# Performance work log

Measured on AMD Instinct MI355X. Metric: run time of the kernel, lower is better.

Reference implementation:

```python
import jax, jax.numpy as jnp
import numpy as np

NUM_COMPONENTS = 8
STRIDE, PADDING, OUTPUT_PADDING, K = 2, 1, 0, 4


def get_comp_mat(n):
    # Cayley-Dickson construction: entry [i, j] = +/- component index of the
    # weight multiplying input component j to produce output component i.
    A = np.array([[0]])
    while A.shape[0] < n:
        m = A.shape[0]
        A = np.vstack([np.hstack([A, -(A + m)]), np.hstack([A + m, A])])
    return A


def setup_inputs() -> dict:
    key = jax.random.key(0)
    k1, k2, k3 = jax.random.split(key, 3)
    B, Cin, Cout, H = 8, 512, 256, 64
    c_in, c_out = Cin // NUM_COMPONENTS, Cout // NUM_COMPONENTS
    x = jax.random.normal(k1, (B, Cin, H, H), jnp.float32)
    # per-component ConvTranspose2d weights, torch layout [C_in, C_out, kH, kW]
    W = jax.random.normal(k2, (NUM_COMPONENTS, c_in, c_out, K, K), jnp.float32) * 0.05
    b = jax.random.normal(k3, (NUM_COMPONENTS, c_out), jnp.float32) * 0.05
    return {"x": x, "W": W, "b": b}


def reference(x, W, b):
    n = NUM_COMPONENTS
    comp = get_comp_mat(n)                 # static [n, n] signed component table
    signs = jnp.asarray(np.where(comp < 0, -1.0, 1.0), x.dtype)
    idx = np.abs(comp)                     # which sub-conv weight to use
    c_in, c_out, kh, kw = W.shape[1:]
    # Fuse the n^2 transpose convs into ONE block transpose conv:
    # Kbig[j*c_in:(j+1)*c_in, i*c_out:(i+1)*c_out] = sign[i,j] * W[idx[i,j]]
    Wsel = W[idx] * signs[:, :, None, None, None, None]          # [ni, nj, c_in, c_out, kh, kw]
    Wbig = jnp.transpose(Wsel, (1, 2, 0, 3, 4, 5)).reshape(n * c_in, n * c_out, kh, kw)
    bbig = jnp.einsum('ij,ijc->ic', signs, b[idx]).reshape(n * c_out)
    # torch ConvTranspose2d == conv with input dilated by stride and flipped kernel
    rhs = jnp.flip(Wbig, (2, 3)).transpose(1, 0, 2, 3)           # OIHW
    pad = K - 1 - PADDING
    out = jax.lax.conv_general_dilated(
        x, rhs, window_strides=(1, 1),
        padding=((pad, pad + OUTPUT_PADDING), (pad, pad + OUTPUT_PADDING)),
        lhs_dilation=(STRIDE, STRIDE),
        dimension_numbers=('NCHW', 'OIHW', 'NCHW'))
    return out + bbig[None, :, None, None]
```

## Files before the change

### kernel.cpp

```cpp
#include <hip/hip_runtime.h>
#include <hip/hip_bf16.h>

typedef unsigned short ushort_t;
typedef __attribute__((ext_vector_type(8))) short short8;
typedef __attribute__((ext_vector_type(4))) float f32x4;

#define NCOMP    8
#define CIN      512
#define COUT     256
#define H        64
#define HP       66
#define OHW      128
#define NB       8

__device__ const int d_idx8[8][8] = {
    {0,1,2,1,4,3,2,3},
    {1,0,3,2,5,4,1,2},
    {2,1,0,1,6,5,4,3},
    {3,2,1,0,7,6,5,4},
    {4,3,2,3,0,1,2,1},
    {5,4,1,2,1,0,3,2},
    {6,5,4,3,2,1,0,1},
    {7,6,5,4,3,2,1,0}};

__device__ const int kh_tab[2][2] = {{1,3},{0,2}};
__device__ const int dh_tab[2][2] = {{0,-1},{1,0}};

__global__ void zero_halo(ushort_t* __restrict__ xpadT) {
    const int t = blockIdx.x * 256 + threadIdx.x;
    const int nA = 8 * 2 * 66 * 64;
    short8 z = {0, 0, 0, 0, 0, 0, 0, 0};
    if (t < nA) {
        int v  = t & 63;
        int r  = t >> 6;
        int iw = r % 66;
        int q  = r / 66;
        int ih = (q & 1) * 65;
        int b  = q >> 1;
        *(short8*)(xpadT + (((size_t)b * HP + ih) * HP + iw) * CIN + v * 8) = z;
    } else {
        int u  = t - nA;
        int v  = u & 63;
        int r  = u >> 6;
        int e  = r & 1;
        int q  = r >> 1;
        int ih = (q & 63) + 1;
        int b  = q >> 6;
        int iw = e * 65;
        *(short8*)(xpadT + (((size_t)b * HP + ih) * HP + iw) * CIN + v * 8) = z;
    }
}

__global__ void prep_x(const float* __restrict__ x, ushort_t* __restrict__ xpadT) {
    __shared__ ushort_t tile[32][33];
    const int ih  = blockIdx.x;
    const int iw0 = (blockIdx.y & 1) * 32;
    const int ic0 = (blockIdx.y >> 1) * 32;
    const int b   = blockIdx.z;
    const int t   = threadIdx.x;

    for (int e = t; e < 1024; e += 256) {
        int icl = e >> 5, iwl = e & 31;
        float v = x[(((size_t)b * CIN + ic0 + icl) * H + ih) * H + iw0 + iwl];
        __hip_bfloat16 h = __float2bfloat16(v);
        tile[icl][iwl] = *(ushort_t*)&h;
    }
    __syncthreads();
    const int iwl = t >> 3, g = t & 7;
    ushort4 v;
    v.x = tile[g * 4 + 0][iwl];
    v.y = tile[g * 4 + 1][iwl];
    v.z = tile[g * 4 + 2][iwl];
    v.w = tile[g * 4 + 3][iwl];
    ushort_t* dst = xpadT + (((size_t)b * HP + ih + 1) * HP + iw0 + iwl + 1) * CIN + ic0 + g * 4;
    *(ushort4*)dst = v;
}

__global__ void prep_w(const float* __restrict__ W, const float* __restrict__ bias,
                       ushort_t* __restrict__ Abf, float* __restrict__ bbig) {
    const int t = blockIdx.x * blockDim.x + threadIdx.x;
    if (t < 4 * 64 * 256 * 32) {
        int kin = t & 31;
        int oc  = (t >> 5) & 255;
        int ks  = (t >> 13) & 63;
        int cls = t >> 19;
        int k  = ks * 32 + kin;
        int a  = k >> 10, c = (k >> 9) & 1, ic = k & 511;
        int ph = cls >> 1, pw = cls & 1;
        int kh = kh_tab[ph][a], kw = kh_tab[pw][c];
        int i = oc >> 5, co = oc & 31;
        int j = ic >> 6, ci = ic & 63;
        float s = (i >= j) ? 1.0f : -1.0f;
        float v = s * W[(((size_t)(d_idx8[i][j] * 64 + ci) * 32 + co) * 4 + kh) * 4 + kw];
        __hip_bfloat16 h = __float2bfloat16(v);
        Abf[t] = *(ushort_t*)&h;
    }
    if (t < COUT) {
        int i = t >> 5, co = t & 31;
        float acc = 0.0f;
        for (int j = 0; j < NCOMP; ++j)
            acc += ((i >= j) ? 1.0f : -1.0f) * bias[d_idx8[i][j] * 32 + co];
        bbig[t] = acc;
    }
}

__device__ __forceinline__ void async16(void* lds_dst, const void* g_src) {
    __builtin_amdgcn_global_load_lds(
        (const __attribute__((address_space(1))) unsigned int*)g_src,
        (__attribute__((address_space(3))) unsigned int*)lds_dst,
        16, 0, 0);
}

#define KSTEP(STEP, CB_CUR, CB_NXT)                                            \
  {                                                                            \
    const int ns = (STEP) + 1;                                                 \
    if (ns < 64) {                                                             \
      const int na  = ns >> 5;                                                 \
      const int ncb = (ns >> 4) & 1;                                           \
      const int go  = ((na ? dh1 : dh0) * HP + (ncb ? dw1 : dw0)) * CIN        \
                      + (ns & 15) * 32;                                        \
      const ushort_t* nap = Abf_t + (size_t)ns * 8192;                         \
      async16(sb + (CB_NXT) + t * 16,         nap);                            \
      async16(sb + (CB_NXT) + 4096 + t * 16,  nap + 2048);                     \
      async16(sb + (CB_NXT) + 8192 + t * 16,  base_r0 + go);                   \
      async16(sb + (CB_NXT) + 12288 + t * 16, base_r1 + go);                   \
    }                                                                          \
    short8 af[4], bf[4];                                                       \
    _Pragma("unroll")                                                          \
    for (int s = 0; s < 4; ++s) {                                              \
      af[s] = *(const short8*)(sb + (CB_CUR) + aoff + s * 1024);               \
      bf[s] = *(const short8*)(sb + (CB_CUR) + boff + s * 1024);               \
    }                                                                          \
    _Pragma("unroll")                                                          \
    for (int sm = 0; sm < 4; ++sm)                                             \
      _Pragma("unroll")                                                        \
      for (int sn = 0; sn < 4; ++sn)                                           \
        acc[sm][sn] = __builtin_amdgcn_mfma_f32_16x16x32_bf16(                 \
            af[sm], bf[sn], acc[sm][sn], 0, 0, 0);                             \
    asm volatile("s_waitcnt vmcnt(0) lgkmcnt(0)" ::: "memory");                \
    __builtin_amdgcn_s_barrier();                                              \
    __builtin_amdgcn_sched_barrier(0);                                         \
  }

__launch_bounds__(256)
__global__ void htconv_mfma(const ushort_t* __restrict__ xpadT,
                            const ushort_t* __restrict__ Abf,
                            const float* __restrict__ bbig,
                            float* __restrict__ out) {
    __shared__ __align__(16) ushort_t smem[16384];
    char* sb = (char*)smem;

    const int t     = threadIdx.x;
    const int ntile = blockIdx.x;
    const int mtile = blockIdx.y;
    const int cls   = blockIdx.z & 3;
    const int b     = blockIdx.z >> 2;
    const int ph = cls >> 1, pw = cls & 1;
    const int ohh0 = ntile * 2;

    const int srcc = (((t & 3) ^ ((t >> 3) & 3)) * 8);
    const int m_a  = t >> 2;
    const ushort_t* Abf_t =
        Abf + (((size_t)cls * 64) * 256 + (size_t)mtile * 128 + m_a) * 32 + srcc;

    const int dh0 = dh_tab[ph][0], dh1 = dh_tab[ph][1];
    const int dw0 = dh_tab[pw][0], dw1 = dh_tab[pw][1];
    const int oww = t >> 2;
    const ushort_t* base_r0 =
        xpadT + (((size_t)b * HP + ohh0 + 0 + 1) * HP + oww + 1) * CIN + srcc;
    const ushort_t* base_r1 =
        xpadT + (((size_t)b * HP + ohh0 + 1 + 1) * HP + oww + 1) * CIN + srcc;

    const int lane = t & 63, wave = t >> 6;
    const int wm = wave >> 1, wn = wave & 1;
    const int col = lane & 15, quad = lane >> 4;
    const int soff = (quad ^ ((col >> 1) & 3)) * 16;
    const int aoff = (wm * 64 + col) * 64 + soff;
    const int boff = 8192 + (wn * 64 + col) * 64 + soff;

    f32x4 acc[4][4];
#pragma unroll
    for (int i = 0; i < 4; ++i)
#pragma unroll
        for (int j = 0; j < 4; ++j)
            acc[i][j] = (f32x4){0.f, 0.f, 0.f, 0.f};

    {
        const int go0 = (dh0 * HP + dw0) * CIN;
        async16(sb + t * 16,         Abf_t);
        async16(sb + 4096 + t * 16,  Abf_t + 2048);
        async16(sb + 8192 + t * 16,  base_r0 + go0);
        async16(sb + 12288 + t * 16, base_r1 + go0);
    }
    asm volatile("s_waitcnt vmcnt(0)" ::: "memory");
    __builtin_amdgcn_s_barrier();
    __builtin_amdgcn_sched_barrier(0);

#pragma unroll 1
    for (int sp = 0; sp < 32; ++sp) {
        KSTEP(2 * sp,     0,     16384);
        KSTEP(2 * sp + 1, 16384, 0);
    }

    const int oh = 2 * (ohh0 + wn) + ph;
#pragma unroll
    for (int sm = 0; sm < 4; ++sm) {
#pragma unroll
        for (int r = 0; r < 4; ++r) {
            const int occ = mtile * 128 + wm * 64 + sm * 16 + quad * 4 + r;
            const float bv = bbig[occ];
            float* obase = out + (((size_t)b * COUT + occ) * OHW + oh) * OHW + pw;
#pragma unroll
            for (int sn = 0; sn < 4; ++sn) {
                const int owi = sn * 16 + col;
                obase[2 * owi] = acc[sm][sn][r] + bv;
            }
        }
    }
}

extern "C" void kernel_launch(void* const* d_in, const int* in_sizes, int n_in,
                              void* d_out, int out_size, void* d_ws, size_t ws_size,
                              hipStream_t stream) {
    const float* x    = (const float*)d_in[0];
    const float* W    = (const float*)d_in[1];
    const float* bias = (const float*)d_in[2];
    float* out = (float*)d_out;

    ushort_t* xpadT = (ushort_t*)d_ws;
    ushort_t* Abf   = xpadT + (size_t)NB * HP * HP * CIN;
    float*    bbig  = (float*)(Abf + (size_t)4 * 64 * 256 * 32);

    zero_halo<<<dim3(520), 256, 0, stream>>>(xpadT);
    prep_x<<<dim3(H, 32, NB), 256, 0, stream>>>(x, xpadT);
    prep_w<<<dim3((4 * 64 * 256 * 32) / 256), 256, 0, stream>>>(W, bias, Abf, bbig);
    htconv_mfma<<<dim3(32, 2, 32), 256, 0, stream>>>(xpadT, Abf, bbig, out);
}
```

Before: 357.2 us.

## Triple-buffer LDS staging with partial vmcnt waits to overlap loads and MFMA

Replaces the double-buffered K loop, which drained all outstanding loads at every step, with a three-stage LDS ring. Each step waits with vmcnt(4), so the next stage's async global-to-LDS loads stay in flight while MFMAs consume the current buffer. This hides global load latency behind compute, at the cost of 48KB of LDS per block, which may reduce occupancy. The lgkmcnt wait before the barrier is dropped; the barrier at the top of each step is relied on to protect buffer reuse.

```diff
diff --git a/kernel.cpp b/kernel.cpp
--- a/kernel.cpp
+++ b/kernel.cpp
@@ -111,25 +111,27 @@
         16, 0, 0);
 }
 
-#define KSTEP(STEP, CB_CUR, CB_NXT)                                            \
+#define STAGE(NS, CB)                                                          \
   {                                                                            \
-    const int ns = (STEP) + 1;                                                 \
-    if (ns < 64) {                                                             \
-      const int na  = ns >> 5;                                                 \
-      const int ncb = (ns >> 4) & 1;                                           \
-      const int go  = ((na ? dh1 : dh0) * HP + (ncb ? dw1 : dw0)) * CIN        \
-                      + (ns & 15) * 32;                                        \
-      const ushort_t* nap = Abf_t + (size_t)ns * 8192;                         \
-      async16(sb + (CB_NXT) + t * 16,         nap);                            \
-      async16(sb + (CB_NXT) + 4096 + t * 16,  nap + 2048);                     \
-      async16(sb + (CB_NXT) + 8192 + t * 16,  base_r0 + go);                   \
-      async16(sb + (CB_NXT) + 12288 + t * 16, base_r1 + go);                   \
-    }                                                                          \
+    const int ns_  = (NS);                                                     \
+    const int na_  = ns_ >> 5;                                                 \
+    const int ncb_ = (ns_ >> 4) & 1;                                           \
+    const int go_  = ((na_ ? dh1 : dh0) * HP + (ncb_ ? dw1 : dw0)) * CIN       \
+                     + (ns_ & 15) * 32;                                        \
+    const ushort_t* nap_ = Abf_t + (size_t)ns_ * 8192;                         \
+    async16(sb + (CB) + t * 16,         nap_);                                 \
+    async16(sb + (CB) + 4096 + t * 16,  nap_ + 2048);                          \
+    async16(sb + (CB) + 8192 + t * 16,  base_r0 + go_);                        \
+    async16(sb + (CB) + 12288 + t * 16, base_r1 + go_);                        \
+  }
+
+#define COMPUTE(CB)                                                            \
+  {                                                                            \
     short8 af[4], bf[4];                                                       \
     _Pragma("unroll")                                                          \
     for (int s = 0; s < 4; ++s) {                                              \
-      af[s] = *(const short8*)(sb + (CB_CUR) + aoff + s * 1024);               \
-      bf[s] = *(const short8*)(sb + (CB_CUR) + boff + s * 1024);               \
+      af[s] = *(const short8*)(sb + (CB) + aoff + s * 1024);                   \
+      bf[s] = *(const short8*)(sb + (CB) + boff + s * 1024);                   \
     }                                                                          \
     _Pragma("unroll")                                                          \
     for (int sm = 0; sm < 4; ++sm)                                             \
@@ -137,17 +139,19 @@
       for (int sn = 0; sn < 4; ++sn)                                           \
         acc[sm][sn] = __builtin_amdgcn_mfma_f32_16x16x32_bf16(                 \
             af[sm], bf[sn], acc[sm][sn], 0, 0, 0);                             \
-    asm volatile("s_waitcnt vmcnt(0) lgkmcnt(0)" ::: "memory");                \
-    __builtin_amdgcn_s_barrier();                                              \
-    __builtin_amdgcn_sched_barrier(0);                                         \
   }
+
+#define WAITBAR(N)                                                             \
+  asm volatile("s_waitcnt vmcnt(" #N ")" ::: "memory");                        \
+  __builtin_amdgcn_s_barrier();                                                \
+  __builtin_amdgcn_sched_barrier(0);
 
 __launch_bounds__(256)
 __global__ void htconv_mfma(const ushort_t* __restrict__ xpadT,
                             const ushort_t* __restrict__ Abf,
                             const float* __restrict__ bbig,
                             float* __restrict__ out) {
-    __shared__ __align__(16) ushort_t smem[16384];
+    __shared__ __align__(16) ushort_t smem[24576];
     char* sb = (char*)smem;
 
     const int t     = threadIdx.x;
@@ -185,22 +189,20 @@
         for (int j = 0; j < 4; ++j)
             acc[i][j] = (f32x4){0.f, 0.f, 0.f, 0.f};
 
-    {
-        const int go0 = (dh0 * HP + dw0) * CIN;
-        async16(sb + t * 16,         Abf_t);
-        async16(sb + 4096 + t * 16,  Abf_t + 2048);
-        async16(sb + 8192 + t * 16,  base_r0 + go0);
-        async16(sb + 12288 + t * 16, base_r1 + go0);
-    }
-    asm volatile("s_waitcnt vmcnt(0)" ::: "memory");
-    __builtin_amdgcn_s_barrier();
-    __builtin_amdgcn_sched_barrier(0);
+    STAGE(0, 0);
+    STAGE(1, 16384);
 
 #pragma unroll 1
-    for (int sp = 0; sp < 32; ++sp) {
-        KSTEP(2 * sp,     0,     16384);
-        KSTEP(2 * sp + 1, 16384, 0);
-    }
+    for (int i = 0; i < 20; ++i) {
+        const int n = 3 * i;
+        WAITBAR(4); STAGE(n + 2, 32768); COMPUTE(0);
+        WAITBAR(4); STAGE(n + 3, 0);     COMPUTE(16384);
+        WAITBAR(4); STAGE(n + 4, 16384); COMPUTE(32768);
+    }
+    WAITBAR(4); STAGE(62, 32768); COMPUTE(0);
+    WAITBAR(4); STAGE(63, 0);     COMPUTE(16384);
+    WAITBAR(4);                   COMPUTE(32768);
+    WAITBAR(0);                   COMPUTE(0);
 
     const int oh = 2 * (ohh0 + wn) + ph;
 #pragma unroll
```

Measured after the change: 341.3 us. 4.4% less time.
